# Optimization experiments

Measured on AMD Instinct MI355X. Metric: run time of the kernel, lower is better.

Reference implementation:

```python
import jax, jax.numpy as jnp
import numpy as np

DIM = 256
DT_REF = 1.0
EPS = 1e-7
GATE_MIN, GATE_MAX = 0.01, 0.99


def _safe_forcing(exp_arg):
    # expm1(z)/z with denominator regularized by sign of real part (matches torch _safe_forcing)
    safe_denom = exp_arg + EPS * jnp.sign(exp_arg.real + EPS)
    return (jnp.exp(exp_arg) - 1.0) / safe_denom


def setup_inputs() -> dict:
    key = jax.random.key(0)
    ks = jax.random.split(key, 12)
    B, T, D = 8, 4096, DIM
    x_mean_seq = jax.random.normal(ks[0], (B, T, D), dtype=jnp.float32)
    dt_seq = jax.random.uniform(ks[1], (B, T), dtype=jnp.float32)
    # GlobalFluxTracker params
    decay_re = jax.random.normal(ks[2], (D,), dtype=jnp.float32) * 0.1 - 1.0
    decay_im = jax.random.normal(ks[3], (D,), dtype=jnp.float32) * 0.1
    W_in = jax.random.normal(ks[4], (2 * D, 2 * D), dtype=jnp.float32) * (1.0 / np.sqrt(2 * D))
    b_in = jnp.zeros((2 * D,), dtype=jnp.float32)
    W_out = jax.random.normal(ks[5], (2 * D, 2 * D), dtype=jnp.float32) * (1.0 / np.sqrt(2 * D))
    b_out = jnp.zeros((2 * D,), dtype=jnp.float32)
    W_gate = jax.random.normal(ks[6], (D, 2 * D), dtype=jnp.float32) * (1.0 / np.sqrt(2 * D))
    b_gate = jnp.zeros((D,), dtype=jnp.float32)
    # TemporalPropagator diagonal generator params
    lam_re = jax.random.normal(ks[7], (D,), dtype=jnp.float32) * 0.01
    lam_im = jax.random.normal(ks[8], (D,), dtype=jnp.float32) * 0.1
    return {
        "x_mean_seq": x_mean_seq, "dt_seq": dt_seq,
        "decay_re": decay_re, "decay_im": decay_im,
        "W_in": W_in, "b_in": b_in, "W_out": W_out, "b_out": b_out,
        "W_gate": W_gate, "b_gate": b_gate,
        "lam_re": lam_re, "lam_im": lam_im,
    }


def reference(x_mean_seq, dt_seq, decay_re, decay_im, W_in, b_in,
              W_out, b_out, W_gate, b_gate, lam_re, lam_im):
    # dt ratio [B,T,1]
    dt_ratio = (dt_seq / DT_REF)[..., None]

    # --- GlobalFluxTracker.get_scan_operators ---
    lam_f = -jax.nn.softplus(decay_re) + 1j * decay_im          # [D] complex64
    exp_arg = lam_f[None, None, :] * dt_ratio                    # [B,T,D]
    decay = jnp.exp(exp_arg)                                     # [B,T,D]
    forcing = _safe_forcing(exp_arg)                             # [B,T,D]

    # _mix_input on real input (imag part is zero)
    x_cat = jnp.concatenate([x_mean_seq, jnp.zeros_like(x_mean_seq)], axis=-1)
    x_in = x_cat @ W_in.T + b_in                                 # [B,T,2D]
    x_re, x_im = jnp.split(x_in, 2, axis=-1)
    x_mixed = x_re + 1j * x_im                                   # [B,T,D]
    X_scan = x_mixed * forcing                                   # [B,T,D]

    # --- linear recurrence flux_t = decay_t * flux_{t-1} + X_t (associative scan over T) ---
    def combine(c1, c2):
        a1, b1 = c1
        a2, b2 = c2
        return (a1 * a2, b1 * a2 + b2)
    _, flux = jax.lax.associative_scan(combine, (decay, X_scan), axis=1)  # [B,T,D]

    # --- compute_output_seq ---
    s_cat = jnp.concatenate([flux.real, flux.imag], axis=-1)     # [B,T,2D]
    src = s_cat @ W_out.T + b_out
    src_re, src_im = jnp.split(src, 2, axis=-1)
    gate = jax.nn.sigmoid(s_cat @ W_gate.T + b_gate)
    gate = gate * (GATE_MAX - GATE_MIN) + GATE_MIN               # [B,T,D]

    # --- TemporalPropagator.get_transition_operators_seq ---
    lam_p = -jax.nn.softplus(lam_re) + 1j * lam_im
    exp_arg_p = lam_p[None, None, :] * dt_ratio
    decay_p = jnp.exp(exp_arg_p)
    forcing_p = _safe_forcing(exp_arg_p)

    out = jnp.concatenate([
        src_re, src_im, gate,
        decay_p.real, decay_p.imag, forcing_p.real, forcing_p.imag,
    ], axis=-1)                                                  # [B,T,7D]
    return out
```

## Files before the change

kernel.cpp:

```cpp
#include <hip/hip_runtime.h>
#include <math.h>

#define DD 256
#define TT 4096
#define NBATCH 8
#define BTOK 32768
#define EPSF 1e-7f

typedef __attribute__((ext_vector_type(4))) float f32x4;
typedef __attribute__((ext_vector_type(8))) short bf16x8;

__device__ __forceinline__ float softplusf(float x) {
  float e = __expf(-fabsf(x));
  return fmaxf(x, 0.f) + __logf(1.f + e);
}
__device__ __forceinline__ float bf2f(unsigned short u) {
  union { unsigned int i; float f; } v; v.i = ((unsigned int)u) << 16; return v.f;
}
__device__ __forceinline__ unsigned short f2bf(float f) {
  union { float f; unsigned int i; } v; v.f = f;
  unsigned int x = v.i;
  unsigned int lsb = (x >> 16) & 1u;
  x += 0x7fffu + lsb;
  return (unsigned short)(x >> 16);
}
__device__ __forceinline__ void decay_forcing(float are, float aim,
    float& dre, float& dim, float& fre, float& fim) {
  float e = __expf(are);
  float s = __sinf(aim), c = __cosf(aim);
  dre = e * c; dim = e * s;
  float sg = (are + EPSF >= 0.f) ? 1.f : -1.f;
  float denr = are + EPSF * sg;
  float deni = aim;
  float inv = __builtin_amdgcn_rcpf(denr * denr + deni * deni);
  float nr = dre - 1.f, ni = dim;
  fre = (nr * denr + ni * deni) * inv;
  fim = (ni * denr - nr * deni) * inv;
}
__device__ __forceinline__ void gl_lds16(const void* g, void* l) {
  __builtin_amdgcn_global_load_lds(
      (const __attribute__((address_space(1))) unsigned int*)g,
      (__attribute__((address_space(3))) unsigned int*)l, 16, 0, 0);
}

__global__ __launch_bounds__(256) void prep(
    const float* __restrict__ x, unsigned short* __restrict__ Xb,
    const float* __restrict__ Win, unsigned short* __restrict__ Wp1,
    const float* __restrict__ Wout, const float* __restrict__ Wgate,
    unsigned short* __restrict__ Wp3)
{
  const int bid = blockIdx.x;
  if (bid < 8192) {
    size_t i = ((size_t)bid * 256 + threadIdx.x) * 4;
    float4 v = *reinterpret_cast<const float4*>(&x[i]);
    ushort4 u;
    u.x = f2bf(v.x); u.y = f2bf(v.y); u.z = f2bf(v.z); u.w = f2bf(v.w);
    *reinterpret_cast<ushort4*>(&Xb[i]) = u;
  } else if (bid < 8704) {
    const int p = bid - 8192;
    const int k = threadIdx.x;
    const int g = p >> 5, r = p & 31;
    const int src = (r < 16) ? (g * 16 + r) : (256 + g * 16 + (r - 16));
    Wp1[(size_t)p * 256 + k] = f2bf(Win[(size_t)src * 512 + k]);
  } else {
    const int p = bid - 8704;
    const float* src = (p < 512) ? (Wout + (size_t)p * 512)
                                 : (Wgate + (size_t)(p - 512) * 512);
    Wp3[(size_t)p * 512 + threadIdx.x] = f2bf(src[threadIdx.x]);
    Wp3[(size_t)p * 512 + threadIdx.x + 256] = f2bf(src[threadIdx.x + 256]);
  }
}

__global__ __launch_bounds__(256) void k1_mfma(
    const unsigned short* __restrict__ Xb,
    const unsigned short* __restrict__ Wp,
    const float* __restrict__ bin, const float* __restrict__ dts,
    const float* __restrict__ decr, const float* __restrict__ deci,
    unsigned int* __restrict__ Xri)
{
  __shared__ __align__(16) unsigned short As[128 * 64];
  __shared__ __align__(16) unsigned short Bs[128 * 64];
  const int bx = blockIdx.x;
  const int wg = (bx & 7) * 128 + (bx >> 3);
  const int mt = wg >> 2, nt = wg & 3;
  const int m0 = mt * 128, n0 = nt * 128;
  const int tid = threadIdx.x;
  const int lane = tid & 63, wid = tid >> 6;
  const int wr = wid >> 1, wc = wid & 1;
  const int l15 = lane & 15, hi = lane >> 4;
  const int lrow = tid >> 3;
  const int sslot = (tid & 7) ^ (lrow & 7);
  f32x4 acc[4][4];
  f32x4 z = {0.f, 0.f, 0.f, 0.f};
#pragma unroll
  for (int i = 0; i < 4; ++i)
#pragma unroll
    for (int j = 0; j < 4; ++j) acc[i][j] = z;

  for (int k0 = 0; k0 < 256; k0 += 64) {
    __syncthreads();
#pragma unroll
    for (int c = 0; c < 4; ++c) {
      gl_lds16(&Xb[(size_t)(m0 + c * 32 + lrow) * 256 + k0 + sslot * 8],
               &As[c * 2048 + tid * 8]);
      gl_lds16(&Wp[(size_t)(n0 + c * 32 + lrow) * 256 + k0 + sslot * 8],
               &Bs[c * 2048 + tid * 8]);
    }
    __syncthreads();
#pragma unroll
    for (int kk = 0; kk < 2; ++kk) {
      bf16x8 af[4], bfr[4];
      const int rslot = ((kk * 4 + hi) ^ (l15 & 7)) * 8;
#pragma unroll
      for (int m = 0; m < 4; ++m)
        af[m] = *reinterpret_cast<const bf16x8*>(&As[(wr * 64 + m * 16 + l15) * 64 + rslot]);
#pragma unroll
      for (int n = 0; n < 4; ++n)
        bfr[n] = *reinterpret_cast<const bf16x8*>(&Bs[(wc * 64 + n * 16 + l15) * 64 + rslot]);
#pragma unroll
      for (int m = 0; m < 4; ++m)
#pragma unroll
        for (int n = 0; n < 4; ++n)
          acc[m][n] = __builtin_amdgcn_mfma_f32_16x16x32_bf16(af[m], bfr[n], acc[m][n], 0, 0, 0);
    }
  }

  const int pbase = n0 + wc * 64;
#pragma unroll
  for (int pr = 0; pr < 2; ++pr) {
    const int d = (pbase >> 1) + pr * 16 + l15;
    const float nre = -softplusf(decr[d]);
    const float di = deci[d];
    const float br = bin[d], bi = bin[d + 256];
#pragma unroll
    for (int m = 0; m < 4; ++m) {
#pragma unroll
      for (int r = 0; r < 4; ++r) {
        const int row = m0 + wr * 64 + m * 16 + hi * 4 + r;
        float xr = acc[m][2 * pr][r] + br;
        float xi = acc[m][2 * pr + 1][r] + bi;
        float dt = dts[row];
        float are = nre * dt, aim = di * dt;
        float dr_, dm_, fr_, fm_;
        decay_forcing(are, aim, dr_, dm_, fr_, fm_);
        unsigned int pk = (unsigned int)f2bf(xr * fr_ - xi * fm_)
                        | ((unsigned int)f2bf(xr * fm_ + xi * fr_) << 16);
        Xri[(size_t)row * DD + d] = pk;
      }
    }
  }
}

__global__ __launch_bounds__(256) void k2a_chunk(
    const unsigned int* __restrict__ Xri,
    const float* __restrict__ dts, const float* __restrict__ decr,
    const float* __restrict__ deci,
    float4* __restrict__ ops)
{
  const int bx = blockIdx.x;
  const int b = bx >> 6, c = bx & 63;
  const int d = threadIdx.x;
  __shared__ float sdt[64];
  if (threadIdx.x < 64) sdt[threadIdx.x] = dts[b * TT + c * 64 + threadIdx.x];
  const float nre = -softplusf(decr[d]);
  const float di = deci[d];
  __syncthreads();
  float Ar = 1.f, Ai = 0.f, Br = 0.f, Bi = 0.f;
  size_t base = (size_t)(b * TT + c * 64) * DD + d;
  for (int i = 0; i < 64; ++i) {
    float dt = sdt[i];
    float e = __expf(nre * dt);
    float s = __sinf(di * dt), cs = __cosf(di * dt);
    float ar = e * cs, ai = e * s;
    unsigned int pk = Xri[base]; base += DD;
    float xr = bf2f((unsigned short)(pk & 0xffffu));
    float xi = bf2f((unsigned short)(pk >> 16));
    float nAr = Ar * ar - Ai * ai, nAi = Ar * ai + Ai * ar;
    Ar = nAr; Ai = nAi;
    float nBr = Br * ar - Bi * ai + xr, nBi = Br * ai + Bi * ar + xi;
    Br = nBr; Bi = nBi;
  }
  ops[(size_t)bx * DD + d] = make_float4(Ar, Ai, Br, Bi);
}

__global__ __launch_bounds__(256) void k2c_apply(
    const unsigned int* __restrict__ Xri,
    const float* __restrict__ dts, const float* __restrict__ decr,
    const float* __restrict__ deci,
    const float4* __restrict__ ops,
    unsigned short* __restrict__ F)
{
  const int bx = blockIdx.x;
  const int b = bx >> 6, c = bx & 63;
  const int d = threadIdx.x;
  __shared__ float sdt[64];
  if (threadIdx.x < 64) sdt[threadIdx.x] = dts[b * TT + c * 64 + threadIdx.x];
  const float nre = -softplusf(decr[d]);
  const float di = deci[d];
  __syncthreads();

  float hr = 0.f, hi2 = 0.f;
  const size_t obase = (size_t)(b * 64) * DD + d;
  for (int c0 = 0; c0 < c; c0 += 8) {
    float4 oo[8];
#pragma unroll
    for (int j = 0; j < 8; ++j)
      oo[j] = (c0 + j < c) ? ops[obase + (size_t)(c0 + j) * DD]
                           : make_float4(1.f, 0.f, 0.f, 0.f);
#pragma unroll
    for (int j = 0; j < 8; ++j) {
      float nr = oo[j].x * hr - oo[j].y * hi2 + oo[j].z;
      float ni = oo[j].x * hi2 + oo[j].y * hr + oo[j].w;
      hr = nr; hi2 = ni;
    }
  }

  const int tok0 = b * TT + c * 64;
  size_t base = (size_t)tok0 * DD + d;
  for (int i = 0; i < 64; ++i) {
    float dt = sdt[i];
    float e = __expf(nre * dt);
    float s = __sinf(di * dt), cs = __cosf(di * dt);
    float ar = e * cs, ai = e * s;
    unsigned int pk = Xri[base]; base += DD;
    float xr = bf2f((unsigned short)(pk & 0xffffu));
    float xi = bf2f((unsigned short)(pk >> 16));
    float nr = ar * hr - ai * hi2 + xr;
    float ni = ar * hi2 + ai * hr + xi;
    hr = nr; hi2 = ni;
    size_t fb = (size_t)(tok0 + i) * 512 + d;
    F[fb] = f2bf(hr);
    F[fb + 256] = f2bf(hi2);
  }
}

__global__ __launch_bounds__(256) void k3k4(
    const unsigned short* __restrict__ F,
    const unsigned short* __restrict__ Wp,
    const float* __restrict__ bout, const float* __restrict__ bgate,
    const float* __restrict__ dts, const float* __restrict__ lre,
    const float* __restrict__ lim,
    float* __restrict__ out)
{
  __shared__ __align__(16) unsigned short As[128 * 64];
  __shared__ __align__(16) unsigned short Bs[128 * 64];

  if (blockIdx.x >= 1536) {
    const int pb = blockIdx.x - 1536;
    const int d = threadIdx.x;
    const float nl = -softplusf(lre[d]);
    const float li = lim[d];
    const int tok0 = pb * 32;
#pragma unroll 4
    for (int i = 0; i < 32; ++i) {
      const int tok = tok0 + i;
      float dt = dts[tok];
      float dr, dm, fr, fm;
      decay_forcing(nl * dt, li * dt, dr, dm, fr, fm);
      float* o = out + (size_t)tok * 1792 + 768;
      o[d] = dr; o[256 + d] = dm; o[512 + d] = fr; o[768 + d] = fm;
    }
    return;
  }

  const int bx = blockIdx.x;
  const int wg = (bx & 7) * 192 + (bx >> 3);
  const int mt = wg / 6, nt = wg % 6;
  const int m0 = mt * 128, n0 = nt * 128;
  const int tid = threadIdx.x;
  const int lane = tid & 63, wid = tid >> 6;
  const int wr = wid >> 1, wc = wid & 1;
  const int l15 = lane & 15, hi = lane >> 4;
  const int lrow = tid >> 3;
  const int sslot = (tid & 7) ^ (lrow & 7);
  f32x4 acc[4][4];
  f32x4 z = {0.f, 0.f, 0.f, 0.f};
#pragma unroll
  for (int i = 0; i < 4; ++i)
#pragma unroll
    for (int j = 0; j < 4; ++j) acc[i][j] = z;

  for (int k0 = 0; k0 < 512; k0 += 64) {
    __syncthreads();
#pragma unroll
    for (int c = 0; c < 4; ++c) {
      gl_lds16(&F[(size_t)(m0 + c * 32 + lrow) * 512 + k0 + sslot * 8],
               &As[c * 2048 + tid * 8]);
      gl_lds16(&Wp[(size_t)(n0 + c * 32 + lrow) * 512 + k0 + sslot * 8],
               &Bs[c * 2048 + tid * 8]);
    }
    __syncthreads();
#pragma unroll
    for (int kk = 0; kk < 2; ++kk) {
      bf16x8 af[4], bfr[4];
      const int rslot = ((kk * 4 + hi) ^ (l15 & 7)) * 8;
#pragma unroll
      for (int m = 0; m < 4; ++m)
        af[m] = *reinterpret_cast<const bf16x8*>(&As[(wr * 64 + m * 16 + l15) * 64 + rslot]);
#pragma unroll
      for (int n = 0; n < 4; ++n)
        bfr[n] = *reinterpret_cast<const bf16x8*>(&Bs[(wc * 64 + n * 16 + l15) * 64 + rslot]);
#pragma unroll
      for (int m = 0; m < 4; ++m)
#pragma unroll
        for (int n = 0; n < 4; ++n)
          acc[m][n] = __builtin_amdgcn_mfma_f32_16x16x32_bf16(af[m], bfr[n], acc[m][n], 0, 0, 0);
    }
  }

  const int nb = n0 + wc * 64;
  if (nb < 512) {
#pragma unroll
    for (int j = 0; j < 4; ++j) {
      const int col = nb + j * 16 + l15;
      const float bb = bout[col];
#pragma unroll
      for (int m = 0; m < 4; ++m)
#pragma unroll
        for (int r = 0; r < 4; ++r) {
          const int row = m0 + wr * 64 + m * 16 + hi * 4 + r;
          out[(size_t)row * 1792 + col] = acc[m][j][r] + bb;
        }
    }
  } else {
#pragma unroll
    for (int j = 0; j < 4; ++j) {
      const int col = nb + j * 16 + l15;
      const float bb = bgate[col - 512];
#pragma unroll
      for (int m = 0; m < 4; ++m)
#pragma unroll
        for (int r = 0; r < 4; ++r) {
          const int row = m0 + wr * 64 + m * 16 + hi * 4 + r;
          float g = __builtin_amdgcn_rcpf(1.f + __expf(-(acc[m][j][r] + bb)));
          out[(size_t)row * 1792 + col] = g * 0.98f + 0.01f;
        }
    }
  }
}

extern "C" void kernel_launch(void* const* d_in, const int* in_sizes, int n_in,
                              void* d_out, int out_size, void* d_ws, size_t ws_size,
                              hipStream_t stream)
{
  const float* x     = (const float*)d_in[0];
  const float* dts   = (const float*)d_in[1];
  const float* decr  = (const float*)d_in[2];
  const float* deci  = (const float*)d_in[3];
  const float* Win   = (const float*)d_in[4];
  const float* bin   = (const float*)d_in[5];
  const float* Wout  = (const float*)d_in[6];
  const float* bout  = (const float*)d_in[7];
  const float* Wgate = (const float*)d_in[8];
  const float* bgate = (const float*)d_in[9];
  const float* lre   = (const float*)d_in[10];
  const float* lim   = (const float*)d_in[11];
  float* out = (float*)d_out;
  char* ws = (char*)d_ws;

  unsigned short* F   = (unsigned short*)(ws);
  unsigned short* Xb  = (unsigned short*)(ws + (size_t)16 * 1024 * 1024);
  unsigned int*  Xri  = (unsigned int*)(ws + (size_t)32 * 1024 * 1024);
  unsigned short* Wp1 = (unsigned short*)(ws + (size_t)64 * 1024 * 1024);
  unsigned short* Wp3 = (unsigned short*)(ws + (size_t)64 * 1024 * 1024 + 262144);
  float4* ops = (float4*)(ws + (size_t)65 * 1024 * 1024);

  prep<<<9472, 256, 0, stream>>>(x, Xb, Win, Wp1, Wout, Wgate, Wp3);
  k1_mfma<<<1024, 256, 0, stream>>>(Xb, Wp1, bin, dts, decr, deci, Xri);
  k2a_chunk<<<512, 256, 0, stream>>>(Xri, dts, decr, deci, ops);
  k2c_apply<<<512, 256, 0, stream>>>(Xri, dts, decr, deci, ops, F);
  k3k4<<<2560, 256, 0, stream>>>(F, Wp3, bout, bgate, dts, lre, lim, out);
}
```

Measured before the change: 136.1 us.

## Fuse bf16 conversion of inputs and weights into GEMM tile loads, drop prep kernel

Removes the separate prep kernel that converted x, W_in, W_out and W_gate to bf16 in workspace. The GEMM kernels now load fp32 tiles directly from global memory into registers, convert them to bf16 and store them into swizzled LDS, with the W_in row permutation computed inline. This saves one launch plus the write and re-read of the bf16 activation copy. In exchange, k1 reads twice as many bytes of x, loses the async global-to-LDS path, and every GEMM block re-converts the weights.

After: 150.8 us. 10.8% more time.

```diff
diff --git a/kernel.cpp b/kernel.cpp
--- a/kernel.cpp
+++ b/kernel.cpp
@@ -23,6 +23,14 @@
   unsigned int lsb = (x >> 16) & 1u;
   x += 0x7fffu + lsb;
   return (unsigned short)(x >> 16);
+}
+__device__ __forceinline__ bf16x8 pack8(const float4& lo, const float4& hi4) {
+  bf16x8 v;
+  v[0] = (short)f2bf(lo.x); v[1] = (short)f2bf(lo.y);
+  v[2] = (short)f2bf(lo.z); v[3] = (short)f2bf(lo.w);
+  v[4] = (short)f2bf(hi4.x); v[5] = (short)f2bf(hi4.y);
+  v[6] = (short)f2bf(hi4.z); v[7] = (short)f2bf(hi4.w);
+  return v;
 }
 __device__ __forceinline__ void decay_forcing(float are, float aim,
     float& dre, float& dim, float& fre, float& fim) {
@@ -43,37 +51,9 @@
       (__attribute__((address_space(3))) unsigned int*)l, 16, 0, 0);
 }
 
-__global__ __launch_bounds__(256) void prep(
-    const float* __restrict__ x, unsigned short* __restrict__ Xb,
-    const float* __restrict__ Win, unsigned short* __restrict__ Wp1,
-    const float* __restrict__ Wout, const float* __restrict__ Wgate,
-    unsigned short* __restrict__ Wp3)
-{
-  const int bid = blockIdx.x;
-  if (bid < 8192) {
-    size_t i = ((size_t)bid * 256 + threadIdx.x) * 4;
-    float4 v = *reinterpret_cast<const float4*>(&x[i]);
-    ushort4 u;
-    u.x = f2bf(v.x); u.y = f2bf(v.y); u.z = f2bf(v.z); u.w = f2bf(v.w);
-    *reinterpret_cast<ushort4*>(&Xb[i]) = u;
-  } else if (bid < 8704) {
-    const int p = bid - 8192;
-    const int k = threadIdx.x;
-    const int g = p >> 5, r = p & 31;
-    const int src = (r < 16) ? (g * 16 + r) : (256 + g * 16 + (r - 16));
-    Wp1[(size_t)p * 256 + k] = f2bf(Win[(size_t)src * 512 + k]);
-  } else {
-    const int p = bid - 8704;
-    const float* src = (p < 512) ? (Wout + (size_t)p * 512)
-                                 : (Wgate + (size_t)(p - 512) * 512);
-    Wp3[(size_t)p * 512 + threadIdx.x] = f2bf(src[threadIdx.x]);
-    Wp3[(size_t)p * 512 + threadIdx.x + 256] = f2bf(src[threadIdx.x + 256]);
-  }
-}
-
 __global__ __launch_bounds__(256) void k1_mfma(
-    const unsigned short* __restrict__ Xb,
-    const unsigned short* __restrict__ Wp,
+    const float* __restrict__ x,
+    const float* __restrict__ Win,
     const float* __restrict__ bin, const float* __restrict__ dts,
     const float* __restrict__ decr, const float* __restrict__ deci,
     unsigned int* __restrict__ Xri)
@@ -90,6 +70,13 @@
   const int l15 = lane & 15, hi = lane >> 4;
   const int lrow = tid >> 3;
   const int sslot = (tid & 7) ^ (lrow & 7);
+  int wrow[4];
+#pragma unroll
+  for (int c = 0; c < 4; ++c) {
+    const int p = n0 + c * 32 + lrow;
+    const int g = p >> 5, r = p & 31;
+    wrow[c] = (r < 16) ? (g * 16 + r) : (256 + g * 16 + (r - 16));
+  }
   f32x4 acc[4][4];
   f32x4 z = {0.f, 0.f, 0.f, 0.f};
 #pragma unroll
@@ -98,13 +85,21 @@
     for (int j = 0; j < 4; ++j) acc[i][j] = z;
 
   for (int k0 = 0; k0 < 256; k0 += 64) {
+    float4 a0[4], a1[4], b0[4], b1[4];
+#pragma unroll
+    for (int c = 0; c < 4; ++c) {
+      const float* ga = &x[(size_t)(m0 + c * 32 + lrow) * 256 + k0 + sslot * 8];
+      a0[c] = *reinterpret_cast<const float4*>(ga);
+      a1[c] = *reinterpret_cast<const float4*>(ga + 4);
+      const float* gb = &Win[(size_t)wrow[c] * 512 + k0 + sslot * 8];
+      b0[c] = *reinterpret_cast<const float4*>(gb);
+      b1[c] = *reinterpret_cast<const float4*>(gb + 4);
+    }
     __syncthreads();
 #pragma unroll
     for (int c = 0; c < 4; ++c) {
-      gl_lds16(&Xb[(size_t)(m0 + c * 32 + lrow) * 256 + k0 + sslot * 8],
-               &As[c * 2048 + tid * 8]);
-      gl_lds16(&Wp[(size_t)(n0 + c * 32 + lrow) * 256 + k0 + sslot * 8],
-               &Bs[c * 2048 + tid * 8]);
+      *reinterpret_cast<bf16x8*>(&As[c * 2048 + tid * 8]) = pack8(a0[c], a1[c]);
+      *reinterpret_cast<bf16x8*>(&Bs[c * 2048 + tid * 8]) = pack8(b0[c], b1[c]);
     }
     __syncthreads();
 #pragma unroll
@@ -236,7 +231,7 @@
 
 __global__ __launch_bounds__(256) void k3k4(
     const unsigned short* __restrict__ F,
-    const unsigned short* __restrict__ Wp,
+    const float* __restrict__ Wout, const float* __restrict__ Wgate,
     const float* __restrict__ bout, const float* __restrict__ bgate,
     const float* __restrict__ dts, const float* __restrict__ lre,
     const float* __restrict__ lim,
@@ -273,6 +268,12 @@
   const int l15 = lane & 15, hi = lane >> 4;
   const int lrow = tid >> 3;
   const int sslot = (tid & 7) ^ (lrow & 7);
+  const float* wsrc[4];
+#pragma unroll
+  for (int c = 0; c < 4; ++c) {
+    const int p = n0 + c * 32 + lrow;
+    wsrc[c] = (p < 512) ? (Wout + (size_t)p * 512) : (Wgate + (size_t)(p - 512) * 512);
+  }
   f32x4 acc[4][4];
   f32x4 z = {0.f, 0.f, 0.f, 0.f};
 #pragma unroll
@@ -281,13 +282,19 @@
     for (int j = 0; j < 4; ++j) acc[i][j] = z;
 
   for (int k0 = 0; k0 < 512; k0 += 64) {
+    float4 b0[4], b1[4];
+#pragma unroll
+    for (int c = 0; c < 4; ++c) {
+      const float* gb = wsrc[c] + k0 + sslot * 8;
+      b0[c] = *reinterpret_cast<const float4*>(gb);
+      b1[c] = *reinterpret_cast<const float4*>(gb + 4);
+    }
     __syncthreads();
 #pragma unroll
     for (int c = 0; c < 4; ++c) {
       gl_lds16(&F[(size_t)(m0 + c * 32 + lrow) * 512 + k0 + sslot * 8],
                &As[c * 2048 + tid * 8]);
-      gl_lds16(&Wp[(size_t)(n0 + c * 32 + lrow) * 512 + k0 + sslot * 8],
-               &Bs[c * 2048 + tid * 8]);
+      *reinterpret_cast<bf16x8*>(&Bs[c * 2048 + tid * 8]) = pack8(b0[c], b1[c]);
     }
     __syncthreads();
 #pragma unroll
@@ -358,16 +365,12 @@
   float* out = (float*)d_out;
   char* ws = (char*)d_ws;
 
-  unsigned short* F   = (unsigned short*)(ws);
-  unsigned short* Xb  = (unsigned short*)(ws + (size_t)16 * 1024 * 1024);
-  unsigned int*  Xri  = (unsigned int*)(ws + (size_t)32 * 1024 * 1024);
-  unsigned short* Wp1 = (unsigned short*)(ws + (size_t)64 * 1024 * 1024);
-  unsigned short* Wp3 = (unsigned short*)(ws + (size_t)64 * 1024 * 1024 + 262144);
-  float4* ops = (float4*)(ws + (size_t)65 * 1024 * 1024);
-
-  prep<<<9472, 256, 0, stream>>>(x, Xb, Win, Wp1, Wout, Wgate, Wp3);
-  k1_mfma<<<1024, 256, 0, stream>>>(Xb, Wp1, bin, dts, decr, deci, Xri);
+  unsigned short* F  = (unsigned short*)(ws);
+  unsigned int* Xri  = (unsigned int*)(ws + (size_t)32 * 1024 * 1024);
+  float4* ops = (float4*)(ws + (size_t)64 * 1024 * 1024);
+
+  k1_mfma<<<1024, 256, 0, stream>>>(x, Win, bin, dts, decr, deci, Xri);
   k2a_chunk<<<512, 256, 0, stream>>>(Xri, dts, decr, deci, ops);
   k2c_apply<<<512, 256, 0, stream>>>(Xri, dts, decr, deci, ops, F);
-  k3k4<<<2560, 256, 0, stream>>>(F, Wp3, bout, bgate, dts, lre, lim, out);
-}
+  k3k4<<<2560, 256, 0, stream>>>(F, Wout, Wgate, bout, bgate, dts, lre, lim, out);
+}
```
